# Optimization experiments

Hardware: AMD Instinct MI355X
Metric: run time of the kernel (lower is better)

## Reference

```python
import jax, jax.numpy as jnp
import numpy as np

B, S, D, O, E, R, TOP_K = 4, 1024, 1024, 1024, 8, 16, 2
SCALING = 32.0 / 16.0  # lora_alpha / r
NEG_INF = -1e9  # stand-in for float('-inf'); exp underflows to 0 identically after softmax shift


def setup_inputs() -> dict:
    key = jax.random.key(0)
    ks = jax.random.split(key, 6)
    return {
        "x": jax.random.normal(ks[0], (B, S, D), jnp.float32),
        "base_w": jax.random.normal(ks[1], (O, D), jnp.float32) * 0.02,
        "base_b": jnp.zeros((O,), jnp.float32),
        "lora_A": jax.random.normal(ks[2], (E, D, R), jnp.float32) * 0.02,
        "lora_B": jax.random.normal(ks[3], (E, R, O), jnp.float32) * 0.02,
        "router_w": jax.random.normal(ks[4], (E, D), jnp.float32) * 0.02,
        "router_b": jnp.zeros((E,), jnp.float32),
    }


def reference(x, base_w, base_b, lora_A, lora_B, router_w, router_b):
    # base layer: F.linear(x, W, b)
    result = jnp.einsum('bsd,od->bso', x, base_w) + base_b
    # per-expert LoRA: ax = x @ A_e, bax = ax @ B_e
    ax = jnp.einsum('bsd,edr->bser', x, lora_A)        # [B,S,E,R]
    bax = jnp.einsum('bser,ero->bseo', ax, lora_B)     # [B,S,E,O]
    # linear router logits
    logits = jnp.einsum('bsd,ed->bse', x, router_w) + router_b  # [B,S,E]
    # top-k routing: mask logits below the k-th largest to -inf
    kth = jax.lax.top_k(logits, TOP_K)[0][..., -1:]
    masked = jnp.where(logits < kth, NEG_INF, logits)
    expert_weights = jax.nn.softmax(masked, axis=-1)   # [B,S,E]
    # combine experts, scale, add to base output
    return result + SCALING * jnp.einsum('bse,bseo->bso', expert_weights, bax)
```

## Files before the change

kernel.cpp:

```cpp
#include <hip/hip_runtime.h>
#include <cmath>

#define M_TOK 4096
#define KD    1024
#define KEXT  1152
#define NOUT  1024
#define ERDIM 128
#define SCALING 2.0f

typedef short bf16x8 __attribute__((ext_vector_type(8)));
typedef float f32x4  __attribute__((ext_vector_type(4)));

__device__ __forceinline__ ushort f2bf(float f) {
    union { float f; unsigned u; } v; v.f = f;
    unsigned r = v.u + 0x7fffu + ((v.u >> 16) & 1u);
    return (ushort)(r >> 16);
}

typedef const unsigned int __attribute__((address_space(1)))* gas_ptr;
typedef unsigned int __attribute__((address_space(3)))* las_ptr;
__device__ __forceinline__ void gld_lds16(const ushort* g, ushort* l) {
    __builtin_amdgcn_global_load_lds((gas_ptr)g, (las_ptr)l, 16, 0, 0);
}

__global__ __launch_bounds__(256) void prep_router(
    const float* __restrict__ x, const float* __restrict__ rw,
    const float* __restrict__ rb, const float* __restrict__ base_w,
    const float* __restrict__ lora_A, const float* __restrict__ lora_B,
    ushort* __restrict__ Aext, ushort* __restrict__ Bext,
    ushort* __restrict__ LAT, float* __restrict__ wgt)
{
    const int tid = threadIdx.x;
    if (blockIdx.x >= 4096) {
        int i = (blockIdx.x - 4096) * 256 + tid;
        const int NB = NOUT * KEXT;
        if (i < NB) {
            int o = i / KEXT;
            int c = i - o * KEXT;
            float v = (c < KD) ? base_w[(size_t)o * KD + c]
                               : lora_B[(size_t)(c - KD) * NOUT + o];
            Bext[i] = f2bf(v);
        } else {
            int j = i - NB;
            int er = j >> 10, d = j & 1023;
            int e = er >> 4, r = er & 15;
            LAT[j] = f2bf(lora_A[((size_t)e * KD + d) * 16 + r]);
        }
        return;
    }
    const int t = blockIdx.x;
    const float4 xv = ((const float4*)(x + (size_t)t * KD))[tid];

    ushort4 xb;
    xb.x = f2bf(xv.x); xb.y = f2bf(xv.y); xb.z = f2bf(xv.z); xb.w = f2bf(xv.w);
    ((ushort4*)(Aext + (size_t)t * KEXT))[tid] = xb;

    double p[8];
    #pragma unroll
    for (int e = 0; e < 8; e++) {
        const float4 wv = ((const float4*)(rw + (size_t)e * KD))[tid];
        p[e] = (double)(xv.x * wv.x) + (double)(xv.y * wv.y) +
               (double)(xv.z * wv.z) + (double)(xv.w * wv.w);
    }
    #pragma unroll
    for (int e = 0; e < 8; e++)
        #pragma unroll
        for (int off = 32; off > 0; off >>= 1)
            p[e] += __shfl_xor(p[e], off);

    __shared__ double red[4][8];
    __shared__ float  lg[8];
    const int wave = tid >> 6, lane = tid & 63;
    if (lane == 0) {
        #pragma unroll
        for (int e = 0; e < 8; e++) red[wave][e] = p[e];
    }
    __syncthreads();
    if (tid < 8) {
        double s = red[0][tid] + red[1][tid] + red[2][tid] + red[3][tid]
                 + (double)rb[tid];
        lg[tid] = (float)s;
    }
    __syncthreads();
    if (tid < 8) {
        float my = lg[tid];
        float m1 = -INFINITY, m2 = -INFINITY;
        #pragma unroll
        for (int i = 0; i < 8; i++) {
            float v = lg[i];
            if (v > m1) { m2 = m1; m1 = v; }
            else if (v > m2) { m2 = v; }
        }
        float denom = 0.f;
        #pragma unroll
        for (int i = 0; i < 8; i++)
            if (lg[i] >= m2) denom += expf(lg[i] - m1);
        float w = (my >= m2) ? expf(my - m1) / denom : 0.f;
        wgt[t * 8 + tid] = SCALING * w;
    }
}

template <int EPI>
__global__ __launch_bounds__(256) void gemm_bt(
    const ushort* __restrict__ A, int lda,
    const ushort* __restrict__ B, int ldb,
    float* __restrict__ C, int ldc,
    const float* __restrict__ bias,
    int k_per_z, int zstride, int ksteps)
{
    __shared__ __attribute__((aligned(16))) ushort As[2][128 * 64];
    __shared__ __attribute__((aligned(16))) ushort Bs[2][128 * 64];

    const int tid  = threadIdx.x;
    const int wave = tid >> 6;
    const int lane = tid & 63;
    const int m0 = blockIdx.x * 128;
    const int n0 = blockIdx.y * 128;
    const int k0 = blockIdx.z * k_per_z;
    C += (size_t)blockIdx.z * zstride;

    const int srow = tid >> 3;
    const int scol = ((tid & 7) ^ (srow & 7)) * 8;
    const ushort* aP = A + (size_t)(m0 + srow) * lda + k0 + scol;
    const ushort* bP = B + (size_t)(n0 + srow) * ldb + k0 + scol;

    const int wr = (wave >> 1) * 64;
    const int wc = (wave & 1) * 64;
    const int fm = lane & 15;
    const int q  = lane >> 4;
    const int rx = fm & 7;

    f32x4 acc[4][4] = {};

    #pragma unroll
    for (int p = 0; p < 4; p++) {
        gld_lds16(aP + (size_t)p * 32 * lda, &As[0][tid * 8 + p * 2048]);
        gld_lds16(bP + (size_t)p * 32 * ldb, &Bs[0][tid * 8 + p * 2048]);
    }

    for (int ks = 0; ks < ksteps; ++ks) {
        __syncthreads();
        if (ks + 1 < ksteps) {
            const int kk = (ks + 1) * 64;
            ushort* a_d = &As[(ks + 1) & 1][0];
            ushort* b_d = &Bs[(ks + 1) & 1][0];
            #pragma unroll
            for (int p = 0; p < 4; p++) {
                gld_lds16(aP + kk + (size_t)p * 32 * lda, a_d + tid * 8 + p * 2048);
                gld_lds16(bP + kk + (size_t)p * 32 * ldb, b_d + tid * 8 + p * 2048);
            }
        }
        const ushort* as = &As[ks & 1][0];
        const ushort* bs = &Bs[ks & 1][0];

        bf16x8 af[2][4], bf[2][4];
        #pragma unroll
        for (int kh = 0; kh < 2; kh++)
            #pragma unroll
            for (int i = 0; i < 4; i++) {
                const int sg = ((kh * 4 + q) ^ rx) * 8;
                af[kh][i] = *(const bf16x8*)&as[(wr + i * 16 + fm) * 64 + sg];
                bf[kh][i] = *(const bf16x8*)&bs[(wc + i * 16 + fm) * 64 + sg];
            }
        #pragma unroll
        for (int kh = 0; kh < 2; kh++)
            #pragma unroll
            for (int mi = 0; mi < 4; mi++)
                #pragma unroll
                for (int ni = 0; ni < 4; ni++)
                    acc[mi][ni] = __builtin_amdgcn_mfma_f32_16x16x32_bf16(
                        af[kh][mi], bf[kh][ni], acc[mi][ni], 0, 0, 0);
    }

    const int rr = q * 4;
    const int cc = fm;
    #pragma unroll
    for (int ni = 0; ni < 4; ni++) {
        const int col = n0 + wc + ni * 16 + cc;
        const float bv = (EPI == 1) ? bias[col] : 0.0f;
        #pragma unroll
        for (int mi = 0; mi < 4; mi++) {
            const int row = m0 + wr + mi * 16 + rr;
            #pragma unroll
            for (int r = 0; r < 4; r++)
                C[(size_t)(row + r) * ldc + col] = acc[mi][ni][r] + bv;
        }
    }
}

__global__ __launch_bounds__(256) void ax_combine(
    const float* __restrict__ part, const float* __restrict__ wgt,
    ushort* __restrict__ Aext)
{
    int i = blockIdx.x * 256 + threadIdx.x;
    const int t = i >> 7, er = i & 127;
    const int SL = M_TOK * ERDIM;
    float s = part[i] + part[i + SL] + part[i + 2 * SL] + part[i + 3 * SL];
    float w = wgt[t * 8 + (er >> 4)];
    Aext[(size_t)t * KEXT + KD + er] = f2bf(s * w);
}

extern "C" void kernel_launch(void* const* d_in, const int* in_sizes, int n_in,
                              void* d_out, int out_size, void* d_ws, size_t ws_size,
                              hipStream_t stream) {
    const float* x        = (const float*)d_in[0];
    const float* base_w   = (const float*)d_in[1];
    const float* base_b   = (const float*)d_in[2];
    const float* lora_A   = (const float*)d_in[3];
    const float* lora_B   = (const float*)d_in[4];
    const float* router_w = (const float*)d_in[5];
    const float* router_b = (const float*)d_in[6];
    float* out = (float*)d_out;

    char* ws = (char*)d_ws;
    ushort* Aext = (ushort*)(ws);
    ushort* Bext = (ushort*)(ws + 9437184);
    ushort* LAT  = (ushort*)(ws + 11796480);
    float*  wgt  = (float*) (ws + 12058624);
    float*  part = (float*) (ws + 12189696);

    prep_router<<<9216, 256, 0, stream>>>(
        x, router_w, router_b, base_w, lora_A, lora_B, Aext, Bext, LAT, wgt);
    gemm_bt<0><<<dim3(32, 1, 4), 256, 0, stream>>>(
        Aext, KEXT, LAT, KD, part, ERDIM, nullptr,
        256, M_TOK * ERDIM, 4);
    ax_combine<<<2048, 256, 0, stream>>>(part, wgt, Aext);
    gemm_bt<1><<<dim3(32, 8, 1), 256, 0, stream>>>(
        Aext, KEXT, Bext, KEXT, out, NOUT, base_b,
        0, 0, 18);
}
```

Measured before the change: 129.6 us.

## Template GEMM on wave count, shrink per-wave M tile to 32 rows

```diff
diff --git a/kernel.cpp b/kernel.cpp
--- a/kernel.cpp
+++ b/kernel.cpp
@@ -100,21 +100,25 @@
     }
 }
 
-template <int EPI>
-__global__ __launch_bounds__(256) void gemm_bt(
+template <int WM, int EPI>
+__global__ __launch_bounds__(WM * 128) void gemm_bt(
     const ushort* __restrict__ A, int lda,
     const ushort* __restrict__ B, int ldb,
     float* __restrict__ C, int ldc,
     const float* __restrict__ bias,
     int k_per_z, int zstride, int ksteps)
 {
-    __shared__ __attribute__((aligned(16))) ushort As[2][128 * 64];
+    constexpr int THREADS = WM * 128;
+    constexpr int TM = WM * 32;
+    constexpr int PB = 8 / WM;
+
+    __shared__ __attribute__((aligned(16))) ushort As[2][TM * 64];
     __shared__ __attribute__((aligned(16))) ushort Bs[2][128 * 64];
 
     const int tid  = threadIdx.x;
     const int wave = tid >> 6;
     const int lane = tid & 63;
-    const int m0 = blockIdx.x * 128;
+    const int m0 = blockIdx.x * TM;
     const int n0 = blockIdx.y * 128;
     const int k0 = blockIdx.z * k_per_z;
     C += (size_t)blockIdx.z * zstride;
@@ -124,48 +128,52 @@
     const ushort* aP = A + (size_t)(m0 + srow) * lda + k0 + scol;
     const ushort* bP = B + (size_t)(n0 + srow) * ldb + k0 + scol;
 
-    const int wr = (wave >> 1) * 64;
+    const int wr = (wave >> 1) * 32;
     const int wc = (wave & 1) * 64;
     const int fm = lane & 15;
     const int q  = lane >> 4;
     const int rx = fm & 7;
 
-    f32x4 acc[4][4] = {};
-
-    #pragma unroll
-    for (int p = 0; p < 4; p++) {
-        gld_lds16(aP + (size_t)p * 32 * lda, &As[0][tid * 8 + p * 2048]);
-        gld_lds16(bP + (size_t)p * 32 * ldb, &Bs[0][tid * 8 + p * 2048]);
-    }
+    f32x4 acc[2][4] = {};
+
+    auto stage = [&](int buf, int kk) {
+        ushort* a_d = &As[buf][tid * 8];
+        ushort* b_d = &Bs[buf][tid * 8];
+        #pragma unroll
+        for (int p = 0; p < 2; p++)
+            gld_lds16(aP + kk + (size_t)(p * 16 * WM) * lda,
+                      a_d + p * THREADS * 8);
+        #pragma unroll
+        for (int p = 0; p < PB; p++)
+            gld_lds16(bP + kk + (size_t)(p * 16 * WM) * ldb,
+                      b_d + p * THREADS * 8);
+    };
+
+    stage(0, 0);
 
     for (int ks = 0; ks < ksteps; ++ks) {
         __syncthreads();
-        if (ks + 1 < ksteps) {
-            const int kk = (ks + 1) * 64;
-            ushort* a_d = &As[(ks + 1) & 1][0];
-            ushort* b_d = &Bs[(ks + 1) & 1][0];
-            #pragma unroll
-            for (int p = 0; p < 4; p++) {
-                gld_lds16(aP + kk + (size_t)p * 32 * lda, a_d + tid * 8 + p * 2048);
-                gld_lds16(bP + kk + (size_t)p * 32 * ldb, b_d + tid * 8 + p * 2048);
-            }
-        }
+        if (ks + 1 < ksteps)
+            stage((ks + 1) & 1, (ks + 1) * 64);
+
         const ushort* as = &As[ks & 1][0];
         const ushort* bs = &Bs[ks & 1][0];
 
-        bf16x8 af[2][4], bf[2][4];
+        bf16x8 af[2][2], bf[2][4];
+        #pragma unroll
+        for (int kh = 0; kh < 2; kh++) {
+            const int sg = ((kh * 4 + q) ^ rx) * 8;
+            #pragma unroll
+            for (int i = 0; i < 2; i++)
+                af[kh][i] = *(const bf16x8*)&as[(wr + i * 16 + fm) * 64 + sg];
+            #pragma unroll
+            for (int i = 0; i < 4; i++)
+                bf[kh][i] = *(const bf16x8*)&bs[(wc + i * 16 + fm) * 64 + sg];
+        }
         #pragma unroll
         for (int kh = 0; kh < 2; kh++)
             #pragma unroll
-            for (int i = 0; i < 4; i++) {
-                const int sg = ((kh * 4 + q) ^ rx) * 8;
-                af[kh][i] = *(const bf16x8*)&as[(wr + i * 16 + fm) * 64 + sg];
-                bf[kh][i] = *(const bf16x8*)&bs[(wc + i * 16 + fm) * 64 + sg];
-            }
-        #pragma unroll
-        for (int kh = 0; kh < 2; kh++)
-            #pragma unroll
-            for (int mi = 0; mi < 4; mi++)
+            for (int mi = 0; mi < 2; mi++)
                 #pragma unroll
                 for (int ni = 0; ni < 4; ni++)
                     acc[mi][ni] = __builtin_amdgcn_mfma_f32_16x16x32_bf16(
@@ -173,13 +181,12 @@
     }
 
     const int rr = q * 4;
-    const int cc = fm;
     #pragma unroll
     for (int ni = 0; ni < 4; ni++) {
-        const int col = n0 + wc + ni * 16 + cc;
+        const int col = n0 + wc + ni * 16 + fm;
         const float bv = (EPI == 1) ? bias[col] : 0.0f;
         #pragma unroll
-        for (int mi = 0; mi < 4; mi++) {
+        for (int mi = 0; mi < 2; mi++) {
             const int row = m0 + wr + mi * 16 + rr;
             #pragma unroll
             for (int r = 0; r < 4; r++)
@@ -221,11 +228,11 @@
 
     prep_router<<<9216, 256, 0, stream>>>(
         x, router_w, router_b, base_w, lora_A, lora_B, Aext, Bext, LAT, wgt);
-    gemm_bt<0><<<dim3(32, 1, 4), 256, 0, stream>>>(
+    gemm_bt<2, 0><<<dim3(64, 1, 4), 256, 0, stream>>>(
         Aext, KEXT, LAT, KD, part, ERDIM, nullptr,
         256, M_TOK * ERDIM, 4);
     ax_combine<<<2048, 256, 0, stream>>>(part, wgt, Aext);
-    gemm_bt<1><<<dim3(32, 8, 1), 256, 0, stream>>>(
+    gemm_bt<4, 1><<<dim3(32, 8, 1), 512, 0, stream>>>(
         Aext, KEXT, Bext, KEXT, out, NOUT, base_b,
         0, 0, 18);
 }
```

Result: faster. 125.5 us (-3.2%).
